# Kernel tuning notes

Hardware: AMD Instinct MI355X
Metric: run time of the kernel (lower is better)

The kernel has to match this reference:

```python
import jax, jax.numpy as jnp
import numpy as np

B, C, H, W = 8, 320, 64, 64      # query feature map
S_KV, D_KV = 77, 1024            # key/value (text) tokens
HEADS, DIM_HEAD = 8, 64
INNER = HEADS * DIM_HEAD         # 512


def setup_inputs() -> dict:
    key = jax.random.key(0)
    ks = jax.random.split(key, 7)
    return {
        "query": jax.random.normal(ks[0], (B, C, H, W), dtype=jnp.float32),
        "key_value": jax.random.normal(ks[1], (B, S_KV, D_KV), dtype=jnp.float32),
        "Wq": jax.random.normal(ks[2], (C, INNER), dtype=jnp.float32) * (C ** -0.5),
        "Wk": jax.random.normal(ks[3], (D_KV, INNER), dtype=jnp.float32) * (D_KV ** -0.5),
        "Wv": jax.random.normal(ks[4], (D_KV, INNER), dtype=jnp.float32) * (D_KV ** -0.5),
        "Wo": jax.random.normal(ks[5], (INNER, C), dtype=jnp.float32) * (INNER ** -0.5),
        "bo": jnp.zeros((C,), dtype=jnp.float32),
    }


def reference(query, key_value, Wq, Wk, Wv, Wo, bo):
    b, c, h, w = query.shape
    n = h * w
    # [B,C,H,W] -> [B,N,C]
    q_flat = query.reshape(b, c, n).transpose(0, 2, 1)
    # projections, then split heads: [B, S, heads, dim_head]
    q = (q_flat @ Wq).reshape(b, n, HEADS, DIM_HEAD)
    k = (key_value @ Wk).reshape(b, S_KV, HEADS, DIM_HEAD)
    v = (key_value @ Wv).reshape(b, S_KV, HEADS, DIM_HEAD)
    scale = DIM_HEAD ** -0.5
    # attn logits: [B, heads, N, S_kv]
    logits = jnp.einsum('bnhd,bshd->bhns', q, k) * scale
    attn = jax.nn.softmax(logits, axis=-1)
    # weighted values -> merge heads: [B, N, inner]
    out = jnp.einsum('bhns,bshd->bnhd', attn, v).reshape(b, n, INNER)
    out = out @ Wo + bo  # dropout p=0.0 is identity
    # [B,N,C] -> [B,C,H,W]
    return out.transpose(0, 2, 1).reshape(b, c, h, w)
```

## Files before the change

kernel.cpp:

```cpp
#include <hip/hip_runtime.h>
#include <hip/hip_bf16.h>
#include <stdint.h>

#define BB     8
#define CC     320
#define NN     4096
#define SKV    77
#define HEADS  8
#define INNER  512
#define SCALE  0.125f

typedef float f32x4  __attribute__((ext_vector_type(4)));
typedef short bf16x8 __attribute__((ext_vector_type(8)));
typedef short s16x4  __attribute__((ext_vector_type(4)));

static __device__ __forceinline__ short f2bf(float f) {
  unsigned u = __float_as_uint(f);
  return (short)((u + 0x7fffu + ((u >> 16) & 1u)) >> 16);
}

static __device__ __forceinline__ void gll16(void* lds, const void* g) {
  auto gp = reinterpret_cast<const uint32_t __attribute__((address_space(1)))*>(
      reinterpret_cast<uintptr_t>(g));
  auto lp = reinterpret_cast<uint32_t __attribute__((address_space(3)))*>(
      reinterpret_cast<uintptr_t>(lds));
  __builtin_amdgcn_global_load_lds(gp, lp, 16, 0, 0);
}

__global__ __launch_bounds__(256) void prep_kernel(
    const float* __restrict__ kv, const float* __restrict__ Wk,
    const float* __restrict__ Wv, const float* __restrict__ Wq,
    const float* __restrict__ Wo, const float* __restrict__ query,
    short* __restrict__ kv_bf, short* __restrict__ Wk_t,
    short* __restrict__ Wv_t, short* __restrict__ Wq_t,
    short* __restrict__ Wo_t, short* __restrict__ X_bf,
    unsigned* __restrict__ zero_base) {
  __shared__ float T[64 * 65];
  const int blk = blockIdx.x, t = threadIdx.x;
  if (blk < 616) {
    const int base = blk * 1024;
    #pragma unroll
    for (int i = 0; i < 4; ++i) kv_bf[base + i*256 + t] = f2bf(kv[base + i*256 + t]);
    return;
  }
  if (blk >= 1392) {
    const int blk2 = blk - 1392;
    const int b = blk2 / 320, r = blk2 % 320;
    const int nt = r / 5, ct = r % 5;
    const int tl = t & 63, rb = t >> 6;
    #pragma unroll
    for (int i = 0; i < 16; ++i) {
      const int c = rb + i*4;
      T[c*65 + tl] = query[((size_t)(b*CC + ct*64 + c))*NN + nt*64 + tl];
    }
    __syncthreads();
    #pragma unroll
    for (int i = 0; i < 16; ++i) {
      const int n = rb + i*4;
      X_bf[((size_t)(b*NN + nt*64 + n))*CC + ct*64 + tl] = f2bf(T[tl*65 + n]);
    }
    return;
  }
  if (blk >= 952) {
    const int base = (blk - 952) * 1024;
    #pragma unroll
    for (int i = 0; i < 4; ++i) zero_base[base + i*256 + t] = 0u;
    return;
  }
  const float* src; short* dst; int RS, CS, kt, ct; float scl = 1.0f;
  if (blk < 872) {
    const int tile = blk - 616;
    const bool isK = tile < 128;
    const int tt = isK ? tile : tile - 128;
    src = isK ? Wk : Wv; dst = isK ? Wk_t : Wv_t;
    RS = 1024; CS = 512; kt = tt >> 3; ct = tt & 7;
  } else if (blk < 912) {
    const int tt = blk - 872;
    src = Wq; dst = Wq_t; RS = 320; CS = 512; kt = tt >> 3; ct = tt & 7;
    scl = SCALE;
  } else {
    const int tt = blk - 912;
    src = Wo; dst = Wo_t; RS = 512; CS = 320; kt = tt / 5; ct = tt % 5;
  }
  const int cl = t & 63, rb = t >> 6;
  #pragma unroll
  for (int i = 0; i < 16; ++i)
    T[(rb + i*4)*65 + cl] = src[(size_t)(kt*64 + rb + i*4)*CS + ct*64 + cl];
  __syncthreads();
  #pragma unroll
  for (int i = 0; i < 16; ++i) {
    const int nl = rb + i*4;
    dst[(size_t)(ct*64 + nl)*RS + kt*64 + cl] = f2bf(T[cl*65 + nl] * scl);
  }
}

__global__ __launch_bounds__(256) void kvproj_kernel(
    const short* __restrict__ kv_bf, const short* __restrict__ Wk_t,
    const short* __restrict__ Wv_t, short* __restrict__ K_ws,
    short* __restrict__ V_ws) {
  const int t = threadIdx.x, w = t >> 6, lane = t & 63;
  const int l15 = lane & 15, q = lane >> 4;
  const int m0 = (blockIdx.x * 4 + w) * 16;
  const int y = blockIdx.y;
  const bool isK = (y < 8);
  const int h = y & 7;
  const short* __restrict__ Wt = isK ? Wk_t : Wv_t;
  const int arow = (m0 + l15 < 616) ? (m0 + l15) : 615;

  const f32x4 z = {0.f, 0.f, 0.f, 0.f};
  f32x4 acc[4] = {z, z, z, z};
  for (int k0 = 0; k0 < 1024; k0 += 32) {
    const bf16x8 a = *(const bf16x8*)(kv_bf + arow*1024 + k0 + q*8);
    #pragma unroll
    for (int nt = 0; nt < 4; ++nt) {
      const int n = h*64 + nt*16 + l15;
      const bf16x8 bfr = *(const bf16x8*)(Wt + n*1024 + k0 + q*8);
      acc[nt] = __builtin_amdgcn_mfma_f32_16x16x32_bf16(a, bfr, acc[nt], 0, 0, 0);
    }
  }
  #pragma unroll
  for (int nt = 0; nt < 4; ++nt) {
    const int d = nt*16 + l15;
    #pragma unroll
    for (int r = 0; r < 4; ++r) {
      const int row = m0 + q*4 + r;
      if (row < 616) {
        const int b = (int)(((unsigned)row * 54472u) >> 22);
        const int s = row - b*77;
        if (isK) K_ws[((b*8 + h)*80 + s)*64 + d] = f2bf(acc[nt][r]);
        else     V_ws[((b*8 + h)*64 + d)*96 + s] = f2bf(acc[nt][r]);
      }
    }
  }
}

__global__ __launch_bounds__(256) void fused_kernel(
    const short* __restrict__ X_bf, const short* __restrict__ Wq_t,
    const short* __restrict__ K_ws, const short* __restrict__ V_ws,
    const short* __restrict__ Wo_t, const float* __restrict__ bo,
    float* __restrict__ out) {
  const int t = threadIdx.x, w = t >> 6, lane = t & 63;
  const int l15 = lane & 15, q = lane >> 4;
  const int b = blockIdx.x >> 6;
  const int n0 = (blockIdx.x & 63) * 64;

  __shared__ short Q_lds[64 * 520];
  __shared__ short STG[26624];

  const f32x4 z = {0.f, 0.f, 0.f, 0.f};

  {
    f32x4 acc[4][8];
    #pragma unroll
    for (int mt = 0; mt < 4; ++mt)
      #pragma unroll
      for (int nt = 0; nt < 8; ++nt) acc[mt][nt] = z;

    const size_t xbase = (size_t)(b * NN + n0) * 320;
    for (int it = 0; it < 10; ++it) {
      const int k0 = it * 32;
      if (it) __syncthreads();
      gll16(STG + t * 8, X_bf + xbase + (size_t)(t >> 2) * 320 + k0 + (t & 3) * 8);
      #pragma unroll
      for (int p = 0; p < 8; ++p) {
        const int f = p * 256 + t, row = f >> 2, c4 = f & 3;
        gll16(STG + 2048 + f * 8, Wq_t + (size_t)row * 320 + k0 + c4 * 8);
      }
      __syncthreads();
      bf16x8 a[4], bb[8];
      #pragma unroll
      for (int mt = 0; mt < 4; ++mt)
        a[mt] = *(const bf16x8*)(STG + (mt * 16 + l15) * 32 + q * 8);
      #pragma unroll
      for (int nt = 0; nt < 8; ++nt)
        bb[nt] = *(const bf16x8*)(STG + 2048 + (w * 128 + nt * 16 + l15) * 32 + q * 8);
      #pragma unroll
      for (int mt = 0; mt < 4; ++mt)
        #pragma unroll
        for (int nt = 0; nt < 8; ++nt)
          acc[mt][nt] = __builtin_amdgcn_mfma_f32_16x16x32_bf16(a[mt], bb[nt], acc[mt][nt], 0, 0, 0);
    }
    #pragma unroll
    for (int mt = 0; mt < 4; ++mt)
      #pragma unroll
      for (int r = 0; r < 4; ++r) {
        const int tok = mt * 16 + q * 4 + r;
        #pragma unroll
        for (int nt = 0; nt < 8; ++nt)
          Q_lds[tok * 520 + w * 128 + nt * 16 + l15] = f2bf(acc[mt][nt][r]);
      }
  }
  __syncthreads();

  {
    short* scrw = STG + w * 6656;
    for (int i = lane; i < 512; i += 64)
      *(unsigned*)(scrw + (i >> 3) * 104 + 80 + (i & 7) * 2) = 0u;

    #pragma unroll
    for (int hh = 0; hh < 2; ++hh) {
      const int h = w * 2 + hh;
      const short* __restrict__ Kh = K_ws + (size_t)(b * 8 + h) * 80 * 64;
      const short* __restrict__ Vh = V_ws + (size_t)(b * 8 + h) * 64 * 96;

      f32x4 qk[4][5];
      #pragma unroll
      for (int nt = 0; nt < 4; ++nt)
        #pragma unroll
        for (int st = 0; st < 5; ++st) qk[nt][st] = z;
      #pragma unroll
      for (int f = 0; f < 2; ++f) {
        bf16x8 bq[4];
        #pragma unroll
        for (int nt = 0; nt < 4; ++nt)
          bq[nt] = *(const bf16x8*)(Q_lds + (nt * 16 + l15) * 520 + h * 64 + f * 32 + q * 8);
        #pragma unroll
        for (int st = 0; st < 5; ++st) {
          const bf16x8 a = *(const bf16x8*)(Kh + (st * 16 + l15) * 64 + f * 32 + q * 8);
          #pragma unroll
          for (int nt = 0; nt < 4; ++nt)
            qk[nt][st] = __builtin_amdgcn_mfma_f32_16x16x32_bf16(a, bq[nt], qk[nt][st], 0, 0, 0);
        }
      }

      #pragma unroll
      for (int nt = 0; nt < 4; ++nt) {
        float mx = -1e30f;
        #pragma unroll
        for (int st = 0; st < 5; ++st)
          #pragma unroll
          for (int r = 0; r < 4; ++r) {
            const int s = st * 16 + q * 4 + r;
            const float vv = (s < SKV) ? qk[nt][st][r] : -1e30f;
            qk[nt][st][r] = vv;
            mx = fmaxf(mx, vv);
          }
        mx = fmaxf(mx, __shfl_xor(mx, 16));
        mx = fmaxf(mx, __shfl_xor(mx, 32));
        float sum = 0.f;
        #pragma unroll
        for (int st = 0; st < 5; ++st)
          #pragma unroll
          for (int r = 0; r < 4; ++r) {
            const int s = st * 16 + q * 4 + r;
            const float e = (s < SKV) ? __expf(qk[nt][st][r] - mx) : 0.f;
            qk[nt][st][r] = e;
            sum += e;
          }
        sum += __shfl_xor(sum, 16);
        sum += __shfl_xor(sum, 32);
        const float inv = 1.0f / sum;
        #pragma unroll
        for (int st = 0; st < 5; ++st) {
          s16x4 pv;
          #pragma unroll
          for (int r = 0; r < 4; ++r) pv[r] = f2bf(qk[nt][st][r] * inv);
          *(s16x4*)(scrw + (nt * 16 + l15) * 104 + st * 16 + q * 4) = pv;
        }
      }

      f32x4 ov[4][4];
      #pragma unroll
      for (int nt = 0; nt < 4; ++nt)
        #pragma unroll
        for (int dt = 0; dt < 4; ++dt) ov[nt][dt] = z;
      #pragma unroll
      for (int f = 0; f < 3; ++f) {
        bf16x8 bp[4];
        #pragma unroll
        for (int nt = 0; nt < 4; ++nt)
          bp[nt] = *(const bf16x8*)(scrw + (nt * 16 + l15) * 104 + f * 32 + q * 8);
        #pragma unroll
        for (int dt = 0; dt < 4; ++dt) {
          const bf16x8 a = *(const bf16x8*)(Vh + (dt * 16 + l15) * 96 + f * 32 + q * 8);
          #pragma unroll
          for (int nt = 0; nt < 4; ++nt)
            ov[nt][dt] = __builtin_amdgcn_mfma_f32_16x16x32_bf16(a, bp[nt], ov[nt][dt], 0, 0, 0);
        }
      }
      #pragma unroll
      for (int nt = 0; nt < 4; ++nt)
        #pragma unroll
        for (int dt = 0; dt < 4; ++dt) {
          s16x4 pv;
          #pragma unroll
          for (int r = 0; r < 4; ++r) pv[r] = f2bf(ov[nt][dt][r]);
          *(s16x4*)(Q_lds + (nt * 16 + l15) * 520 + h * 64 + dt * 16 + q * 4) = pv;
        }
    }
  }
  __syncthreads();

  {
    f32x4 oc[5][4];
    #pragma unroll
    for (int mt = 0; mt < 5; ++mt)
      #pragma unroll
      for (int nt = 0; nt < 4; ++nt) oc[mt][nt] = z;

    for (int it = 0; it < 16; ++it) {
      const int k0 = it * 32;
      if (it) __syncthreads();
      #pragma unroll
      for (int p = 0; p < 5; ++p) {
        const int f = p * 256 + t, row = f >> 2, c4 = f & 3;
        gll16(STG + f * 8, Wo_t + (size_t)row * 512 + k0 + c4 * 8);
      }
      __syncthreads();
      bf16x8 a[5], bb[4];
      #pragma unroll
      for (int mt = 0; mt < 5; ++mt)
        a[mt] = *(const bf16x8*)(STG + (w * 80 + mt * 16 + l15) * 32 + q * 8);
      #pragma unroll
      for (int nt = 0; nt < 4; ++nt)
        bb[nt] = *(const bf16x8*)(Q_lds + (nt * 16 + l15) * 520 + k0 + q * 8);
      #pragma unroll
      for (int mt = 0; mt < 5; ++mt)
        #pragma unroll
        for (int nt = 0; nt < 4; ++nt)
          oc[mt][nt] = __builtin_amdgcn_mfma_f32_16x16x32_bf16(a[mt], bb[nt], oc[mt][nt], 0, 0, 0);
    }
    #pragma unroll
    for (int mt = 0; mt < 5; ++mt)
      #pragma unroll
      for (int r = 0; r < 4; ++r) {
        const int c = w * 80 + mt * 16 + q * 4 + r;
        const float bv = bo[c];
        float* rowp = out + ((size_t)(b * CC + c)) * NN + n0;
        #pragma unroll
        for (int nt = 0; nt < 4; ++nt)
          rowp[nt * 16 + l15] = oc[mt][nt][r] + bv;
      }
  }
}

extern "C" void kernel_launch(void* const* d_in, const int* in_sizes, int n_in,
                              void* d_out, int out_size, void* d_ws, size_t ws_size,
                              hipStream_t stream) {
  const float* query = (const float*)d_in[0];
  const float* kv    = (const float*)d_in[1];
  const float* Wq    = (const float*)d_in[2];
  const float* Wk    = (const float*)d_in[3];
  const float* Wv    = (const float*)d_in[4];
  const float* Wv_   = (const float*)d_in[4];
  const float* Wo    = (const float*)d_in[5];
  const float* bo    = (const float*)d_in[6];
  (void)Wv_;
  float* out = (float*)d_out;

  char* p = (char*)d_ws;
  short* K_ws  = (short*)(p);
  short* V_ws  = (short*)(p +   819200);
  short* Wq_t  = (short*)(p +  1802240);
  short* Wo_t  = (short*)(p +  2129920);
  short* X_bf  = (short*)(p +  2457600);
  short* kv_bf = (short*)(p + 23429120);
  short* Wk_t  = (short*)(p + 24690688);
  short* Wv_t  = (short*)(p + 25739264);

  prep_kernel<<<3952, 256, 0, stream>>>(kv, Wk, Wv, Wq, Wo, query, kv_bf,
                                        Wk_t, Wv_t, Wq_t, Wo_t, X_bf,
                                        (unsigned*)p);
  kvproj_kernel<<<dim3(10, 16), 256, 0, stream>>>(kv_bf, Wk_t, Wv_t, K_ws, V_ws);
  fused_kernel<<<512, 256, 0, stream>>>(X_bf, Wq_t, K_ws, V_ws, Wo_t, bo, out);
}
```

Baseline: 195.4 us.

## Fuse query transpose and bf16 cast into attention kernel with 32-token tiles

```diff
diff --git a/kernel.cpp b/kernel.cpp
--- a/kernel.cpp
+++ b/kernel.cpp
@@ -19,21 +19,12 @@
   return (short)((u + 0x7fffu + ((u >> 16) & 1u)) >> 16);
 }
 
-static __device__ __forceinline__ void gll16(void* lds, const void* g) {
-  auto gp = reinterpret_cast<const uint32_t __attribute__((address_space(1)))*>(
-      reinterpret_cast<uintptr_t>(g));
-  auto lp = reinterpret_cast<uint32_t __attribute__((address_space(3)))*>(
-      reinterpret_cast<uintptr_t>(lds));
-  __builtin_amdgcn_global_load_lds(gp, lp, 16, 0, 0);
-}
-
 __global__ __launch_bounds__(256) void prep_kernel(
     const float* __restrict__ kv, const float* __restrict__ Wk,
     const float* __restrict__ Wv, const float* __restrict__ Wq,
-    const float* __restrict__ Wo, const float* __restrict__ query,
-    short* __restrict__ kv_bf, short* __restrict__ Wk_t,
-    short* __restrict__ Wv_t, short* __restrict__ Wq_t,
-    short* __restrict__ Wo_t, short* __restrict__ X_bf,
+    const float* __restrict__ Wo, short* __restrict__ kv_bf,
+    short* __restrict__ Wk_t, short* __restrict__ Wv_t,
+    short* __restrict__ Wq_t, short* __restrict__ Wo_t,
     unsigned* __restrict__ zero_base) {
   __shared__ float T[64 * 65];
   const int blk = blockIdx.x, t = threadIdx.x;
@@ -41,24 +32,6 @@
     const int base = blk * 1024;
     #pragma unroll
     for (int i = 0; i < 4; ++i) kv_bf[base + i*256 + t] = f2bf(kv[base + i*256 + t]);
-    return;
-  }
-  if (blk >= 1392) {
-    const int blk2 = blk - 1392;
-    const int b = blk2 / 320, r = blk2 % 320;
-    const int nt = r / 5, ct = r % 5;
-    const int tl = t & 63, rb = t >> 6;
-    #pragma unroll
-    for (int i = 0; i < 16; ++i) {
-      const int c = rb + i*4;
-      T[c*65 + tl] = query[((size_t)(b*CC + ct*64 + c))*NN + nt*64 + tl];
-    }
-    __syncthreads();
-    #pragma unroll
-    for (int i = 0; i < 16; ++i) {
-      const int n = rb + i*4;
-      X_bf[((size_t)(b*NN + nt*64 + n))*CC + ct*64 + tl] = f2bf(T[tl*65 + n]);
-    }
     return;
   }
   if (blk >= 952) {
@@ -134,54 +107,69 @@
   }
 }
 
-__global__ __launch_bounds__(256) void fused_kernel(
-    const short* __restrict__ X_bf, const short* __restrict__ Wq_t,
+__global__ __launch_bounds__(256, 2) void fused_kernel(
+    const float* __restrict__ query, const short* __restrict__ Wq_t,
     const short* __restrict__ K_ws, const short* __restrict__ V_ws,
     const short* __restrict__ Wo_t, const float* __restrict__ bo,
     float* __restrict__ out) {
   const int t = threadIdx.x, w = t >> 6, lane = t & 63;
   const int l15 = lane & 15, q = lane >> 4;
-  const int b = blockIdx.x >> 6;
-  const int n0 = (blockIdx.x & 63) * 64;
-
-  __shared__ short Q_lds[64 * 520];
-  __shared__ short STG[26624];
+  const int b = blockIdx.x >> 7;
+  const int n0 = (blockIdx.x & 127) * 32;
+
+  __shared__ __align__(16) short Q_lds[32 * 520];
+  __shared__ __align__(16) short U[13312];
 
   const f32x4 z = {0.f, 0.f, 0.f, 0.f};
 
   {
-    f32x4 acc[4][8];
-    #pragma unroll
-    for (int mt = 0; mt < 4; ++mt)
+    const float* qb = query + (size_t)b * CC * NN + n0;
+    #pragma unroll
+    for (int i = 0; i < 10; ++i) {
+      const int f = i * 256 + t;
+      const int c = f >> 3, n4 = (f & 7) * 4;
+      const f32x4 v = *(const f32x4*)(qb + (size_t)c * NN + n4);
+      #pragma unroll
+      for (int j = 0; j < 4; ++j)
+        U[(n4 + j) * 328 + c] = f2bf(v[j]);
+    }
+  }
+  __syncthreads();
+
+  {
+    f32x4 acc[2][8];
+    #pragma unroll
+    for (int mt = 0; mt < 2; ++mt)
       #pragma unroll
       for (int nt = 0; nt < 8; ++nt) acc[mt][nt] = z;
 
-    const size_t xbase = (size_t)(b * NN + n0) * 320;
+    const short* __restrict__ Wb = Wq_t + (size_t)(w * 128) * 320;
+    auto ld1 = [&](int it, bf16x8 (&A)[2], bf16x8 (&B)[8]) {
+      const int k0 = it * 32;
+      #pragma unroll
+      for (int x = 0; x < 2; ++x)
+        A[x] = *(const bf16x8*)(U + (x * 16 + l15) * 328 + k0 + q * 8);
+      #pragma unroll
+      for (int x = 0; x < 8; ++x)
+        B[x] = *(const bf16x8*)(Wb + (size_t)(x * 16 + l15) * 320 + k0 + q * 8);
+    };
+    bf16x8 aP[2], bP[8], aN[2], bN[8];
+    ld1(0, aP, bP);
+    #pragma unroll
     for (int it = 0; it < 10; ++it) {
-      const int k0 = it * 32;
-      if (it) __syncthreads();
-      gll16(STG + t * 8, X_bf + xbase + (size_t)(t >> 2) * 320 + k0 + (t & 3) * 8);
-      #pragma unroll
-      for (int p = 0; p < 8; ++p) {
-        const int f = p * 256 + t, row = f >> 2, c4 = f & 3;
-        gll16(STG + 2048 + f * 8, Wq_t + (size_t)row * 320 + k0 + c4 * 8);
-      }
-      __syncthreads();
-      bf16x8 a[4], bb[8];
-      #pragma unroll
-      for (int mt = 0; mt < 4; ++mt)
-        a[mt] = *(const bf16x8*)(STG + (mt * 16 + l15) * 32 + q * 8);
-      #pragma unroll
-      for (int nt = 0; nt < 8; ++nt)
-        bb[nt] = *(const bf16x8*)(STG + 2048 + (w * 128 + nt * 16 + l15) * 32 + q * 8);
-      #pragma unroll
-      for (int mt = 0; mt < 4; ++mt)
+      if (it + 1 < 10) ld1(it + 1, aN, bN);
+      #pragma unroll
+      for (int mt = 0; mt < 2; ++mt)
         #pragma unroll
         for (int nt = 0; nt < 8; ++nt)
-          acc[mt][nt] = __builtin_amdgcn_mfma_f32_16x16x32_bf16(a[mt], bb[nt], acc[mt][nt], 0, 0, 0);
-    }
-    #pragma unroll
-    for (int mt = 0; mt < 4; ++mt)
+          acc[mt][nt] = __builtin_amdgcn_mfma_f32_16x16x32_bf16(aP[mt], bP[nt], acc[mt][nt], 0, 0, 0);
+      #pragma unroll
+      for (int x = 0; x < 2; ++x) aP[x] = aN[x];
+      #pragma unroll
+      for (int x = 0; x < 8; ++x) bP[x] = bN[x];
+    }
+    #pragma unroll
+    for (int mt = 0; mt < 2; ++mt)
       #pragma unroll
       for (int r = 0; r < 4; ++r) {
         const int tok = mt * 16 + q * 4 + r;
@@ -193,8 +181,8 @@
   __syncthreads();
 
   {
-    short* scrw = STG + w * 6656;
-    for (int i = lane; i < 512; i += 64)
+    short* scrw = U + w * 3328;
+    for (int i = lane; i < 256; i += 64)
       *(unsigned*)(scrw + (i >> 3) * 104 + 80 + (i & 7) * 2) = 0u;
 
     #pragma unroll
@@ -203,28 +191,28 @@
       const short* __restrict__ Kh = K_ws + (size_t)(b * 8 + h) * 80 * 64;
       const short* __restrict__ Vh = V_ws + (size_t)(b * 8 + h) * 64 * 96;
 
-      f32x4 qk[4][5];
-      #pragma unroll
-      for (int nt = 0; nt < 4; ++nt)
+      f32x4 qk[2][5];
+      #pragma unroll
+      for (int nt = 0; nt < 2; ++nt)
         #pragma unroll
         for (int st = 0; st < 5; ++st) qk[nt][st] = z;
       #pragma unroll
       for (int f = 0; f < 2; ++f) {
-        bf16x8 bq[4];
-        #pragma unroll
-        for (int nt = 0; nt < 4; ++nt)
+        bf16x8 bq[2];
+        #pragma unroll
+        for (int nt = 0; nt < 2; ++nt)
           bq[nt] = *(const bf16x8*)(Q_lds + (nt * 16 + l15) * 520 + h * 64 + f * 32 + q * 8);
         #pragma unroll
         for (int st = 0; st < 5; ++st) {
           const bf16x8 a = *(const bf16x8*)(Kh + (st * 16 + l15) * 64 + f * 32 + q * 8);
           #pragma unroll
-          for (int nt = 0; nt < 4; ++nt)
+          for (int nt = 0; nt < 2; ++nt)
             qk[nt][st] = __builtin_amdgcn_mfma_f32_16x16x32_bf16(a, bq[nt], qk[nt][st], 0, 0, 0);
         }
       }
 
       #pragma unroll
-      for (int nt = 0; nt < 4; ++nt) {
+      for (int nt = 0; nt < 2; ++nt) {
         float mx = -1e30f;
         #pragma unroll
         for (int st = 0; st < 5; ++st)
@@ -259,27 +247,27 @@
         }
       }
 
-      f32x4 ov[4][4];
-      #pragma unroll
-      for (int nt = 0; nt < 4; ++nt)
+      f32x4 ov[2][4];
+      #pragma unroll
+      for (int nt = 0; nt < 2; ++nt)
         #pragma unroll
         for (int dt = 0; dt < 4; ++dt) ov[nt][dt] = z;
       #pragma unroll
       for (int f = 0; f < 3; ++f) {
-        bf16x8 bp[4];
-        #pragma unroll
-        for (int nt = 0; nt < 4; ++nt)
+        bf16x8 bp[2];
+        #pragma unroll
+        for (int nt = 0; nt < 2; ++nt)
           bp[nt] = *(const bf16x8*)(scrw + (nt * 16 + l15) * 104 + f * 32 + q * 8);
         #pragma unroll
         for (int dt = 0; dt < 4; ++dt) {
           const bf16x8 a = *(const bf16x8*)(Vh + (dt * 16 + l15) * 96 + f * 32 + q * 8);
           #pragma unroll
-          for (int nt = 0; nt < 4; ++nt)
+          for (int nt = 0; nt < 2; ++nt)
             ov[nt][dt] = __builtin_amdgcn_mfma_f32_16x16x32_bf16(a, bp[nt], ov[nt][dt], 0, 0, 0);
         }
       }
       #pragma unroll
-      for (int nt = 0; nt < 4; ++nt)
+      for (int nt = 0; nt < 2; ++nt)
         #pragma unroll
         for (int dt = 0; dt < 4; ++dt) {
           s16x4 pv;
@@ -292,33 +280,36 @@
   __syncthreads();
 
   {
-    f32x4 oc[5][4];
+    f32x4 oc[5][2];
     #pragma unroll
     for (int mt = 0; mt < 5; ++mt)
       #pragma unroll
-      for (int nt = 0; nt < 4; ++nt) oc[mt][nt] = z;
-
+      for (int nt = 0; nt < 2; ++nt) oc[mt][nt] = z;
+
+    const short* __restrict__ Wa = Wo_t + (size_t)(w * 80) * 512;
+    auto ld3 = [&](int it, bf16x8 (&A)[5], bf16x8 (&B)[2]) {
+      const int k0 = it * 32;
+      #pragma unroll
+      for (int x = 0; x < 5; ++x)
+        A[x] = *(const bf16x8*)(Wa + (size_t)(x * 16 + l15) * 512 + k0 + q * 8);
+      #pragma unroll
+      for (int x = 0; x < 2; ++x)
+        B[x] = *(const bf16x8*)(Q_lds + (x * 16 + l15) * 520 + k0 + q * 8);
+    };
+    bf16x8 aP[5], bP[2], aN[5], bN[2];
+    ld3(0, aP, bP);
+    #pragma unroll
     for (int it = 0; it < 16; ++it) {
-      const int k0 = it * 32;
-      if (it) __syncthreads();
-      #pragma unroll
-      for (int p = 0; p < 5; ++p) {
-        const int f = p * 256 + t, row = f >> 2, c4 = f & 3;
-        gll16(STG + f * 8, Wo_t + (size_t)row * 512 + k0 + c4 * 8);
-      }
-      __syncthreads();
-      bf16x8 a[5], bb[4];
+      if (it + 1 < 16) ld3(it + 1, aN, bN);
       #pragma unroll
       for (int mt = 0; mt < 5; ++mt)
-        a[mt] = *(const bf16x8*)(STG + (w * 80 + mt * 16 + l15) * 32 + q * 8);
-      #pragma unroll
-      for (int nt = 0; nt < 4; ++nt)
-        bb[nt] = *(const bf16x8*)(Q_lds + (nt * 16 + l15) * 520 + k0 + q * 8);
-      #pragma unroll
-      for (int mt = 0; mt < 5; ++mt)
-        #pragma unroll
-        for (int nt = 0; nt < 4; ++nt)
-          oc[mt][nt] = __builtin_amdgcn_mfma_f32_16x16x32_bf16(a[mt], bb[nt], oc[mt][nt], 0, 0, 0);
+        #pragma unroll
+        for (int nt = 0; nt < 2; ++nt)
+          oc[mt][nt] = __builtin_amdgcn_mfma_f32_16x16x32_bf16(aP[mt], bP[nt], oc[mt][nt], 0, 0, 0);
+      #pragma unroll
+      for (int x = 0; x < 5; ++x) aP[x] = aN[x];
+      #pragma unroll
+      for (int x = 0; x < 2; ++x) bP[x] = bN[x];
     }
     #pragma unroll
     for (int mt = 0; mt < 5; ++mt)
@@ -328,7 +319,7 @@
         const float bv = bo[c];
         float* rowp = out + ((size_t)(b * CC + c)) * NN + n0;
         #pragma unroll
-        for (int nt = 0; nt < 4; ++nt)
+        for (int nt = 0; nt < 2; ++nt)
           rowp[nt * 16 + l15] = oc[mt][nt][r] + bv;
       }
   }
@@ -342,10 +333,8 @@
   const float* Wq    = (const float*)d_in[2];
   const float* Wk    = (const float*)d_in[3];
   const float* Wv    = (const float*)d_in[4];
-  const float* Wv_   = (const float*)d_in[4];
   const float* Wo    = (const float*)d_in[5];
   const float* bo    = (const float*)d_in[6];
-  (void)Wv_;
   float* out = (float*)d_out;
 
   char* p = (char*)d_ws;
@@ -353,14 +342,13 @@
   short* V_ws  = (short*)(p +   819200);
   short* Wq_t  = (short*)(p +  1802240);
   short* Wo_t  = (short*)(p +  2129920);
-  short* X_bf  = (short*)(p +  2457600);
-  short* kv_bf = (short*)(p + 23429120);
-  short* Wk_t  = (short*)(p + 24690688);
-  short* Wv_t  = (short*)(p + 25739264);
-
-  prep_kernel<<<3952, 256, 0, stream>>>(kv, Wk, Wv, Wq, Wo, query, kv_bf,
-                                        Wk_t, Wv_t, Wq_t, Wo_t, X_bf,
-                                        (unsigned*)p);
+  short* kv_bf = (short*)(p +  2457600);
+  short* Wk_t  = (short*)(p +  3719168);
+  short* Wv_t  = (short*)(p +  4767744);
+
+  prep_kernel<<<1192, 256, 0, stream>>>(kv, Wk, Wv, Wq, Wo, kv_bf,
+                                        Wk_t, Wv_t, Wq_t, Wo_t,
+                                        (unsigned*)V_ws);
   kvproj_kernel<<<dim3(10, 16), 256, 0, stream>>>(kv_bf, Wk_t, Wv_t, K_ws, V_ws);
-  fused_kernel<<<512, 256, 0, stream>>>(X_bf, Wq_t, K_ws, V_ws, Wo_t, bo, out);
-}
+  fused_kernel<<<1024, 256, 0, stream>>>(query, Wq_t, K_ws, V_ws, Wo_t, bo, out);
+}
```

Result: slower. 211.3 us (+8.1%).
